# Kernel optimization log

Measured on AMD Instinct MI355X. Metric: run time of the kernel, lower is better.

The kernel has to match this reference:

```python
import jax, jax.numpy as jnp
import numpy as np

N = 100000
E = 1600000
NFEAT, NHID, NCLASS = 500, 128, 40


def setup_inputs() -> dict:
    key = jax.random.key(0)
    ks = jax.random.split(key, 12)
    x = jax.random.normal(ks[0], (N, NFEAT), dtype=jnp.float32)
    row = jax.random.randint(ks[1], (E,), 0, N, dtype=jnp.int32)
    col = jax.random.randint(ks[2], (E,), 0, N, dtype=jnp.int32)
    # precomputed normalized adjacency values (D^-1/2 A D^-1/2 style)
    edge_weight = jax.random.uniform(ks[3], (E,), dtype=jnp.float32) / 16.0
    def lin(k, fi, fo):
        s = 1.0 / np.sqrt(fi)
        return jax.random.uniform(k, (fi, fo), dtype=jnp.float32, minval=-s, maxval=s)
    return {
        "x": x, "row": row, "col": col, "edge_weight": edge_weight,
        "W1": lin(ks[4], NFEAT, NHID), "b1": jnp.zeros((NHID,), jnp.float32),
        "W2": lin(ks[5], NHID, NHID), "b2": jnp.zeros((NHID,), jnp.float32),
        "W3": lin(ks[6], NHID, NHID), "b3": jnp.zeros((NHID,), jnp.float32),
        "W4": lin(ks[7], NHID, NCLASS), "b4": jnp.zeros((NCLASS,), jnp.float32),
    }


def gcn_layer(h, row, col, edge_weight, W, b):
    # support = h @ W ; out = spmm(adj, support) + b  (Kipf GraphConvolution)
    support = h @ W                                   # [N, Fout]
    msgs = edge_weight[:, None] * support[col]        # [E, Fout] gather on source nodes
    agg = jax.ops.segment_sum(msgs, row, num_segments=N)  # scatter-add to dest nodes
    return agg + b


def reference(x, row, col, edge_weight, W1, b1, W2, b2, W3, b3, W4, b4):
    # dropout is identity in eval mode (training=False)
    h = jax.nn.relu(gcn_layer(x, row, col, edge_weight, W1, b1))
    h = jax.nn.relu(gcn_layer(h, row, col, edge_weight, W2, b2))
    h = jax.nn.relu(gcn_layer(h, row, col, edge_weight, W3, b3))
    h = gcn_layer(h, row, col, edge_weight, W4, b4)
    return jax.nn.log_softmax(h, axis=1)
```

## Files before the change

### kernel.cpp

```cpp
#include <hip/hip_runtime.h>
#include <cstdint>
#include <cstddef>

#define NFEAT 500
#define NHID  128
#define NCLASS 40

typedef __attribute__((ext_vector_type(8))) short bf16x8;
typedef __attribute__((ext_vector_type(4))) float f32x4;

__device__ __forceinline__ unsigned short f2bf(float f) {
    union { float f; unsigned u; } v; v.f = f;
    unsigned u = v.u;
    unsigned r = u + 0x7FFF + ((u >> 16) & 1);
    return (unsigned short)(r >> 16);
}
__device__ __forceinline__ float bf2f(unsigned short h) {
    union { unsigned u; float f; } v; v.u = ((unsigned)h) << 16; return v.f;
}


__global__ void k_hist(const int* __restrict__ row, int E, int* __restrict__ counts) {
    int i = blockIdx.x * 256 + threadIdx.x;
    if (i < E) atomicAdd(&counts[row[i]], 1);
}

__global__ void k_block_sum(const int* __restrict__ counts, int n, int* __restrict__ partials) {
    __shared__ int tmp[256];
    int i = blockIdx.x * 256 + threadIdx.x;
    tmp[threadIdx.x] = (i < n) ? counts[i] : 0;
    __syncthreads();
    for (int o = 128; o > 0; o >>= 1) {
        if (threadIdx.x < o) tmp[threadIdx.x] += tmp[threadIdx.x + o];
        __syncthreads();
    }
    if (threadIdx.x == 0) partials[blockIdx.x] = tmp[0];
}

__global__ void k_scan_partials(int* __restrict__ partials, int nb) {
    __shared__ int tmp[512];
    int t = threadIdx.x;
    int v = (t < nb) ? partials[t] : 0;
    tmp[t] = v;
    __syncthreads();
    for (int o = 1; o < 512; o <<= 1) {
        int add = (t >= o) ? tmp[t - o] : 0;
        __syncthreads();
        tmp[t] += add;
        __syncthreads();
    }
    if (t < nb) partials[t] = tmp[t] - v;
}

__global__ void k_scan_counts(int* __restrict__ counts, const int* __restrict__ partials,
                              int* __restrict__ row_ptr, int n) {
    __shared__ int tmp[256];
    int t = threadIdx.x;
    int i = blockIdx.x * 256 + t;
    int v = (i < n) ? counts[i] : 0;
    tmp[t] = v;
    __syncthreads();
    for (int o = 1; o < 256; o <<= 1) {
        int add = (t >= o) ? tmp[t - o] : 0;
        __syncthreads();
        tmp[t] += add;
        __syncthreads();
    }
    int incl = tmp[t];
    int base = partials[blockIdx.x];
    if (i < n) {
        row_ptr[i] = base + incl - v;
        counts[i] = 0;
    }
    if (i == n - 1) row_ptr[n] = base + incl;
}

__global__ void k_scatter(const int* __restrict__ row, const int* __restrict__ col,
                          const float* __restrict__ w, int E,
                          const int* __restrict__ row_ptr, int* __restrict__ cursor,
                          uint2* __restrict__ csr_cw) {
    int i = blockIdx.x * 256 + threadIdx.x;
    if (i < E) {
        int r = row[i];
        int p = row_ptr[r] + atomicAdd(&cursor[r], 1);
        csr_cw[p] = make_uint2((unsigned)col[i], __float_as_uint(w[i]));
    }
}


__global__ void k_prep_w(const float* __restrict__ W, unsigned short* __restrict__ Wt,
                         int K, int Norig, int Nt, int Kpad) {
    int idx = blockIdx.x * 256 + threadIdx.x;
    if (idx >= Nt * Kpad) return;
    int n = idx / Kpad, k = idx % Kpad;
    unsigned short v = 0;
    if (k < K && n < Norig) v = f2bf(W[(size_t)k * Norig + n]);
    Wt[idx] = v;
}


template<bool AFP32, int BN, int CN, int CPITCH>
__global__ __launch_bounds__(256) void k_gemm_mfma(const void* __restrict__ Ain,
                                                   const unsigned short* __restrict__ Wt,
                                                   unsigned short* __restrict__ C,
                                                   int M, int K, int Kpad) {
    constexpr int P  = 40;
    constexpr int NW = (BN == 128) ? 2 : 1;
    constexpr int MW = 4 / NW;
    constexpr int TM = 64 / (MW * 16);
    constexpr int TN = BN / (NW * 16);
    constexpr int WCH = (BN == 128) ? 2 : 1;
    __shared__ unsigned short As[64][P];
    __shared__ unsigned short Ws[BN][P];

    const int t = threadIdx.x;
    const int lane = t & 63;
    const int w = t >> 6;
    const int wm = w / NW, wn = w % NW;
    const int mbase = blockIdx.x * 64;
    const int l15 = lane & 15, quad = lane >> 4;

    const float* Af = (const float*)Ain;
    const unsigned short* Ab = (const unsigned short*)Ain;

    f32x4 acc[TM][TN];
#pragma unroll
    for (int mi = 0; mi < TM; mi++)
#pragma unroll
        for (int ni = 0; ni < TN; ni++)
            acc[mi][ni] = (f32x4){0.f, 0.f, 0.f, 0.f};

    float4 ra_f[2];
    uint4  ra_b;
    uint4  rw[WCH];

    auto loadA = [&](int k0) {
        if (AFP32) {
#pragma unroll
            for (int p = 0; p < 2; p++) {
                int idx = p * 256 + t;
                int m = idx >> 3, ch = idx & 7;
                int gm = mbase + m, gk = k0 + ch * 4;
                float4 v = make_float4(0.f, 0.f, 0.f, 0.f);
                if (gm < M && gk < K) v = *(const float4*)(Af + (size_t)gm * K + gk);
                ra_f[p] = v;
            }
        } else {
            int m = t >> 2, ch = t & 3;
            ra_b = *(const uint4*)(Ab + (size_t)(mbase + m) * Kpad + k0 + ch * 8);
        }
    };
    auto loadW = [&](int k0) {
#pragma unroll
        for (int p = 0; p < WCH; p++) {
            int idx = p * 256 + t;
            if (BN * 4 > idx) {
                int n = idx >> 2, ch = idx & 3;
                rw[p] = *(const uint4*)(Wt + (size_t)n * Kpad + k0 + ch * 8);
            }
        }
    };
    auto storeLDS = [&]() {
        if (AFP32) {
#pragma unroll
            for (int p = 0; p < 2; p++) {
                int idx = p * 256 + t;
                int m = idx >> 3, ch = idx & 7;
                float4 v = ra_f[p];
                unsigned long long pk = (unsigned long long)f2bf(v.x)
                                      | ((unsigned long long)f2bf(v.y) << 16)
                                      | ((unsigned long long)f2bf(v.z) << 32)
                                      | ((unsigned long long)f2bf(v.w) << 48);
                *(unsigned long long*)&As[m][ch * 4] = pk;
            }
        } else {
            int m = t >> 2, ch = t & 3;
            *(uint4*)&As[m][ch * 8] = ra_b;
        }
#pragma unroll
        for (int p = 0; p < WCH; p++) {
            int idx = p * 256 + t;
            if (BN * 4 > idx) {
                int n = idx >> 2, ch = idx & 3;
                *(uint4*)&Ws[n][ch * 8] = rw[p];
            }
        }
    };

    loadA(0);
    loadW(0);
    for (int k0 = 0; k0 < Kpad; k0 += 32) {
        storeLDS();
        __syncthreads();
        bool more = (k0 + 32) < Kpad;
        if (more) {
            loadA(k0 + 32);
            loadW(k0 + 32);
        }
        bf16x8 afr[TM], bfr[TN];
#pragma unroll
        for (int mi = 0; mi < TM; mi++)
            afr[mi] = *(const bf16x8*)&As[wm * (TM * 16) + mi * 16 + l15][quad * 8];
#pragma unroll
        for (int ni = 0; ni < TN; ni++)
            bfr[ni] = *(const bf16x8*)&Ws[wn * (TN * 16) + ni * 16 + l15][quad * 8];
#pragma unroll
        for (int mi = 0; mi < TM; mi++)
#pragma unroll
            for (int ni = 0; ni < TN; ni++)
                acc[mi][ni] = __builtin_amdgcn_mfma_f32_16x16x32_bf16(afr[mi], bfr[ni], acc[mi][ni], 0, 0, 0);
        if (more) __syncthreads();
    }

#pragma unroll
    for (int mi = 0; mi < TM; mi++) {
#pragma unroll
        for (int r = 0; r < 4; r++) {
            int gm = mbase + wm * (TM * 16) + mi * 16 + quad * 4 + r;
#pragma unroll
            for (int ni = 0; ni < TN; ni++) {
                int gn = wn * (TN * 16) + ni * 16 + l15;
                if (gn < CN) C[(size_t)gm * CPITCH + gn] = f2bf(acc[mi][ni][r]);
            }
        }
    }
}


__global__ __launch_bounds__(256) void k_spmm128(const unsigned short* __restrict__ S,
                                                 const int* __restrict__ rp,
                                                 const uint2* __restrict__ cw,
                                                 const float* __restrict__ bias,
                                                 unsigned short* __restrict__ out,
                                                 int n, int do_relu) {
    int wid  = threadIdx.x >> 6;
    int lane = threadIdx.x & 63;
    int node = blockIdx.x * 4 + wid;
    if (node >= n) return;
    int s = rp[node], e = rp[node + 1];
    float a0x = 0.f, a0y = 0.f, a1x = 0.f, a1y = 0.f;
    float a2x = 0.f, a2y = 0.f, a3x = 0.f, a3y = 0.f;
    int i = s;
    for (; i + 4 <= e; i += 4) {
        uint2 e0 = cw[i], e1 = cw[i + 1], e2 = cw[i + 2], e3 = cw[i + 3];
        unsigned v0 = ((const unsigned*)(S + (size_t)e0.x * NHID))[lane];
        unsigned v1 = ((const unsigned*)(S + (size_t)e1.x * NHID))[lane];
        unsigned v2 = ((const unsigned*)(S + (size_t)e2.x * NHID))[lane];
        unsigned v3 = ((const unsigned*)(S + (size_t)e3.x * NHID))[lane];
        float w0 = __uint_as_float(e0.y), w1 = __uint_as_float(e1.y);
        float w2 = __uint_as_float(e2.y), w3 = __uint_as_float(e3.y);
        a0x = fmaf(w0, bf2f((unsigned short)v0), a0x); a0y = fmaf(w0, bf2f((unsigned short)(v0 >> 16)), a0y);
        a1x = fmaf(w1, bf2f((unsigned short)v1), a1x); a1y = fmaf(w1, bf2f((unsigned short)(v1 >> 16)), a1y);
        a2x = fmaf(w2, bf2f((unsigned short)v2), a2x); a2y = fmaf(w2, bf2f((unsigned short)(v2 >> 16)), a2y);
        a3x = fmaf(w3, bf2f((unsigned short)v3), a3x); a3y = fmaf(w3, bf2f((unsigned short)(v3 >> 16)), a3y);
    }
    for (; i < e; i++) {
        uint2 e0 = cw[i];
        unsigned v0 = ((const unsigned*)(S + (size_t)e0.x * NHID))[lane];
        float w0 = __uint_as_float(e0.y);
        a0x = fmaf(w0, bf2f((unsigned short)v0), a0x); a0y = fmaf(w0, bf2f((unsigned short)(v0 >> 16)), a0y);
    }
    float ax = (a0x + a1x) + (a2x + a3x) + bias[lane * 2];
    float ay = (a0y + a1y) + (a2y + a3y) + bias[lane * 2 + 1];
    if (do_relu) {
        ax = fmaxf(ax, 0.f);
        ay = fmaxf(ay, 0.f);
    }
    unsigned o = (unsigned)f2bf(ax) | ((unsigned)f2bf(ay) << 16);
    __builtin_nontemporal_store(o, (unsigned*)(out + (size_t)node * NHID) + lane);
}


__global__ __launch_bounds__(256) void k_spmm40_lsm(const unsigned short* __restrict__ S,
                                                    const int* __restrict__ rp,
                                                    const uint2* __restrict__ cw,
                                                    const float* __restrict__ bias,
                                                    float* __restrict__ out,
                                                    int n) {
    int wid  = threadIdx.x >> 6;
    int lane = threadIdx.x & 63;
    int node = blockIdx.x * 4 + wid;
    if (node >= n) return;
    int s = rp[node], e = rp[node + 1];
    float a0 = 0.f, a1 = 0.f, a2 = 0.f, a3 = 0.f;
    int i = s;
    bool act = lane < NCLASS;
    for (; i + 4 <= e; i += 4) {
        uint2 e0 = cw[i], e1 = cw[i + 1], e2 = cw[i + 2], e3 = cw[i + 3];
        if (act) {
            float v0 = bf2f(S[(size_t)e0.x * NCLASS + lane]);
            float v1 = bf2f(S[(size_t)e1.x * NCLASS + lane]);
            float v2 = bf2f(S[(size_t)e2.x * NCLASS + lane]);
            float v3 = bf2f(S[(size_t)e3.x * NCLASS + lane]);
            a0 = fmaf(__uint_as_float(e0.y), v0, a0);
            a1 = fmaf(__uint_as_float(e1.y), v1, a1);
            a2 = fmaf(__uint_as_float(e2.y), v2, a2);
            a3 = fmaf(__uint_as_float(e3.y), v3, a3);
        }
    }
    for (; i < e; i++) {
        uint2 e0 = cw[i];
        if (act) a0 = fmaf(__uint_as_float(e0.y), bf2f(S[(size_t)e0.x * NCLASS + lane]), a0);
    }
    float acc = (a0 + a1) + (a2 + a3);
    float logit = act ? acc + bias[lane] : -INFINITY;
    float m = logit;
#pragma unroll
    for (int o = 32; o >= 1; o >>= 1) m = fmaxf(m, __shfl_xor(m, o, 64));
    float ex = act ? expf(logit - m) : 0.f;
    float ssum = ex;
#pragma unroll
    for (int o = 32; o >= 1; o >>= 1) ssum += __shfl_xor(ssum, o, 64);
    if (act) {
        float r = logit - m - logf(ssum);
        __builtin_nontemporal_store(r, out + (size_t)node * NCLASS + lane);
    }
}


extern "C" void kernel_launch(void* const* d_in, const int* in_sizes, int n_in,
                              void* d_out, int out_size, void* d_ws, size_t ws_size,
                              hipStream_t stream) {
    const float* x  = (const float*)d_in[0];
    const int* row  = (const int*)d_in[1];
    const int* col  = (const int*)d_in[2];
    const float* ew = (const float*)d_in[3];
    const float* W1 = (const float*)d_in[4];
    const float* b1 = (const float*)d_in[5];
    const float* W2 = (const float*)d_in[6];
    const float* b2 = (const float*)d_in[7];
    const float* W3 = (const float*)d_in[8];
    const float* b3 = (const float*)d_in[9];
    const float* W4 = (const float*)d_in[10];
    const float* b4 = (const float*)d_in[11];
    float* out = (float*)d_out;

    const int Nn = in_sizes[0] / NFEAT;
    const int E  = in_sizes[1];
    const int NB = (Nn + 255) / 256;
    const int Mpad = (Nn + 63) & ~63;

    char* ws = (char*)d_ws;
    size_t off = 0;
    auto alloc = [&](size_t bytes) {
        size_t o = off;
        off = (off + bytes + 255) & ~(size_t)255;
        return o;
    };
    int*   row_ptr  = (int*)(ws + alloc((size_t)(Nn + 1) * 4));
    int*   counts   = (int*)(ws + alloc((size_t)Nn * 4));
    int*   partials = (int*)(ws + alloc((size_t)NB * 4));
    uint2* csr_cw   = (uint2*)(ws + alloc((size_t)E * 8));
    unsigned short* Sb  = (unsigned short*)(ws + alloc((size_t)Mpad * NHID * 2));
    unsigned short* Hb  = (unsigned short*)(ws + alloc((size_t)Mpad * NHID * 2));
    unsigned short* S4b = (unsigned short*)(ws + alloc((size_t)Mpad * NCLASS * 2));
    unsigned short* Wt1 = (unsigned short*)(ws + alloc((size_t)128 * 512 * 2));
    unsigned short* Wt2 = (unsigned short*)(ws + alloc((size_t)128 * 128 * 2));
    unsigned short* Wt3 = (unsigned short*)(ws + alloc((size_t)128 * 128 * 2));
    unsigned short* Wt4 = (unsigned short*)(ws + alloc((size_t)48 * 128 * 2));

    k_prep_w<<<(128 * 512 + 255) / 256, 256, 0, stream>>>(W1, Wt1, NFEAT, NHID, 128, 512);
    k_prep_w<<<(128 * 128 + 255) / 256, 256, 0, stream>>>(W2, Wt2, NHID, NHID, 128, 128);
    k_prep_w<<<(128 * 128 + 255) / 256, 256, 0, stream>>>(W3, Wt3, NHID, NHID, 128, 128);
    k_prep_w<<<(48 * 128 + 255) / 256, 256, 0, stream>>>(W4, Wt4, NHID, NCLASS, 48, 128);

    (void)hipMemsetAsync(counts, 0, (size_t)Nn * 4, stream);
    k_hist<<<(E + 255) / 256, 256, 0, stream>>>(row, E, counts);
    k_block_sum<<<NB, 256, 0, stream>>>(counts, Nn, partials);
    k_scan_partials<<<1, 512, 0, stream>>>(partials, NB);
    k_scan_counts<<<NB, 256, 0, stream>>>(counts, partials, row_ptr, Nn);
    k_scatter<<<(E + 255) / 256, 256, 0, stream>>>(row, col, ew, E, row_ptr, counts, csr_cw);

    const int gblocks = Mpad / 64;
    const int spmm_blocks = (Nn + 3) / 4;

    k_gemm_mfma<true, 128, 128, 128><<<gblocks, 256, 0, stream>>>(x, Wt1, Sb, Nn, NFEAT, 512);
    k_spmm128<<<spmm_blocks, 256, 0, stream>>>(Sb, row_ptr, csr_cw, b1, Hb, Nn, 1);
    k_gemm_mfma<false, 128, 128, 128><<<gblocks, 256, 0, stream>>>(Hb, Wt2, Sb, Nn, NHID, NHID);
    k_spmm128<<<spmm_blocks, 256, 0, stream>>>(Sb, row_ptr, csr_cw, b2, Hb, Nn, 1);
    k_gemm_mfma<false, 128, 128, 128><<<gblocks, 256, 0, stream>>>(Hb, Wt3, Sb, Nn, NHID, NHID);
    k_spmm128<<<spmm_blocks, 256, 0, stream>>>(Sb, row_ptr, csr_cw, b3, Hb, Nn, 1);
    k_gemm_mfma<false, 48, 40, 40><<<gblocks, 256, 0, stream>>>(Hb, Wt4, S4b, Nn, NHID, NHID);
    k_spmm40_lsm<<<spmm_blocks, 256, 0, stream>>>(S4b, row_ptr, csr_cw, b4, out, Nn);
}
```

Before: 900.8 us.

## Enlarge GEMM M-tile to 128, double-buffer A in LDS, read weights from global

The MFMA GEMM now computes 128 rows per block instead of 64, stages only the A tile in LDS with double buffering, and loads the weight fragments straight from global memory (cached) rather than through LDS. Only one barrier per K step remains, and the stage-2 store overlaps with compute. The aim is to spend less LDS traffic and sync per output and to amortise weight loads over more rows. In exchange each block holds more accumulator registers and fewer blocks are launched, and the direct weight loads add global-memory latency to the inner loop. The fp32 bounds check is also tightened to require the full float4 to be in range.

```diff
diff --git a/kernel.cpp b/kernel.cpp
--- a/kernel.cpp
+++ b/kernel.cpp
@@ -107,17 +107,15 @@
     constexpr int P  = 40;
     constexpr int NW = (BN == 128) ? 2 : 1;
     constexpr int MW = 4 / NW;
-    constexpr int TM = 64 / (MW * 16);
+    constexpr int TM = 128 / (MW * 16);
     constexpr int TN = BN / (NW * 16);
-    constexpr int WCH = (BN == 128) ? 2 : 1;
-    __shared__ unsigned short As[64][P];
-    __shared__ unsigned short Ws[BN][P];
+    __shared__ unsigned short As[2][128][P];
 
     const int t = threadIdx.x;
     const int lane = t & 63;
     const int w = t >> 6;
     const int wm = w / NW, wn = w % NW;
-    const int mbase = blockIdx.x * 64;
+    const int mbase = blockIdx.x * 128;
     const int l15 = lane & 15, quad = lane >> 4;
 
     const float* Af = (const float*)Ain;
@@ -130,40 +128,33 @@
         for (int ni = 0; ni < TN; ni++)
             acc[mi][ni] = (f32x4){0.f, 0.f, 0.f, 0.f};
 
-    float4 ra_f[2];
-    uint4  ra_b;
-    uint4  rw[WCH];
+    float4 ra_f[4];
+    uint4  ra_b[2];
 
     auto loadA = [&](int k0) {
         if (AFP32) {
 #pragma unroll
-            for (int p = 0; p < 2; p++) {
+            for (int p = 0; p < 4; p++) {
                 int idx = p * 256 + t;
                 int m = idx >> 3, ch = idx & 7;
                 int gm = mbase + m, gk = k0 + ch * 4;
                 float4 v = make_float4(0.f, 0.f, 0.f, 0.f);
-                if (gm < M && gk < K) v = *(const float4*)(Af + (size_t)gm * K + gk);
+                if (gm < M && gk + 4 <= K) v = *(const float4*)(Af + (size_t)gm * K + gk);
                 ra_f[p] = v;
             }
         } else {
-            int m = t >> 2, ch = t & 3;
-            ra_b = *(const uint4*)(Ab + (size_t)(mbase + m) * Kpad + k0 + ch * 8);
+#pragma unroll
+            for (int p = 0; p < 2; p++) {
+                int idx = p * 256 + t;
+                int m = idx >> 2, ch = idx & 3;
+                ra_b[p] = *(const uint4*)(Ab + (size_t)(mbase + m) * Kpad + k0 + ch * 8);
+            }
         }
     };
-    auto loadW = [&](int k0) {
-#pragma unroll
-        for (int p = 0; p < WCH; p++) {
-            int idx = p * 256 + t;
-            if (BN * 4 > idx) {
-                int n = idx >> 2, ch = idx & 3;
-                rw[p] = *(const uint4*)(Wt + (size_t)n * Kpad + k0 + ch * 8);
-            }
-        }
-    };
-    auto storeLDS = [&]() {
+    auto storeLDS = [&](int buf) {
         if (AFP32) {
 #pragma unroll
-            for (int p = 0; p < 2; p++) {
+            for (int p = 0; p < 4; p++) {
                 int idx = p * 256 + t;
                 int m = idx >> 3, ch = idx & 7;
                 float4 v = ra_f[p];
@@ -171,45 +162,49 @@
                                       | ((unsigned long long)f2bf(v.y) << 16)
                                       | ((unsigned long long)f2bf(v.z) << 32)
                                       | ((unsigned long long)f2bf(v.w) << 48);
-                *(unsigned long long*)&As[m][ch * 4] = pk;
+                *(unsigned long long*)&As[buf][m][ch * 4] = pk;
             }
         } else {
-            int m = t >> 2, ch = t & 3;
-            *(uint4*)&As[m][ch * 8] = ra_b;
-        }
-#pragma unroll
-        for (int p = 0; p < WCH; p++) {
-            int idx = p * 256 + t;
-            if (BN * 4 > idx) {
-                int n = idx >> 2, ch = idx & 3;
-                *(uint4*)&Ws[n][ch * 8] = rw[p];
+#pragma unroll
+            for (int p = 0; p < 2; p++) {
+                int idx = p * 256 + t;
+                int m = idx >> 2, ch = idx & 3;
+                *(uint4*)&As[buf][m][ch * 8] = ra_b[p];
             }
         }
     };
 
+    const int nIter = Kpad >> 5;
     loadA(0);
-    loadW(0);
-    for (int k0 = 0; k0 < Kpad; k0 += 32) {
-        storeLDS();
-        __syncthreads();
-        bool more = (k0 + 32) < Kpad;
-        if (more) {
-            loadA(k0 + 32);
-            loadW(k0 + 32);
-        }
-        bf16x8 afr[TM], bfr[TN];
+    storeLDS(0);
+    __syncthreads();
+
+    for (int it = 0; it < nIter; it++) {
+        const int cur = it & 1;
+        const int k0 = it << 5;
+        const bool more = (it + 1) < nIter;
+        if (more) loadA(k0 + 32);
+
+        bf16x8 bfr[TN];
+#pragma unroll
+        for (int ni = 0; ni < TN; ni++)
+            bfr[ni] = *(const bf16x8*)(Wt + (size_t)(wn * (TN * 16) + ni * 16 + l15) * Kpad + k0 + quad * 8);
+
+        bf16x8 afr[TM];
 #pragma unroll
         for (int mi = 0; mi < TM; mi++)
-            afr[mi] = *(const bf16x8*)&As[wm * (TM * 16) + mi * 16 + l15][quad * 8];
-#pragma unroll
-        for (int ni = 0; ni < TN; ni++)
-            bfr[ni] = *(const bf16x8*)&Ws[wn * (TN * 16) + ni * 16 + l15][quad * 8];
+            afr[mi] = *(const bf16x8*)&As[cur][wm * (TM * 16) + mi * 16 + l15][quad * 8];
+
 #pragma unroll
         for (int mi = 0; mi < TM; mi++)
 #pragma unroll
             for (int ni = 0; ni < TN; ni++)
                 acc[mi][ni] = __builtin_amdgcn_mfma_f32_16x16x32_bf16(afr[mi], bfr[ni], acc[mi][ni], 0, 0, 0);
-        if (more) __syncthreads();
+
+        if (more) {
+            storeLDS(cur ^ 1);
+            __syncthreads();
+        }
     }
 
 #pragma unroll
@@ -338,7 +333,7 @@
     const int Nn = in_sizes[0] / NFEAT;
     const int E  = in_sizes[1];
     const int NB = (Nn + 255) / 256;
-    const int Mpad = (Nn + 63) & ~63;
+    const int Mpad = (Nn + 127) & ~127;
 
     char* ws = (char*)d_ws;
     size_t off = 0;
@@ -371,7 +366,7 @@
     k_scan_counts<<<NB, 256, 0, stream>>>(counts, partials, row_ptr, Nn);
     k_scatter<<<(E + 255) / 256, 256, 0, stream>>>(row, col, ew, E, row_ptr, counts, csr_cw);
 
-    const int gblocks = Mpad / 64;
+    const int gblocks = Mpad / 128;
     const int spmm_blocks = (Nn + 3) / 4;
 
     k_gemm_mfma<true, 128, 128, 128><<<gblocks, 256, 0, stream>>>(x, Wt1, Sb, Nn, NFEAT, 512);
```

After: 860.1 us. -4.5%, faster.
